# Kernel optimization log

Hardware: AMD Instinct MI355X
Metric: run time of the kernel (lower is better)

The kernel has to match this reference:

```python
import jax, jax.numpy as jnp
import numpy as np

N, T, SKEP = 4096, 64, 768   # users, max history length, SKEP embed dim
H = 256                      # senti_size (LSTM hidden, user_vec/cluster_center dim)
K = 64                       # number of roles (clusters)
NH, DH, DV = 8, 32, 32       # MHA heads, d, d_v


def setup_inputs() -> dict:
    key = jax.random.key(0)
    ks = jax.random.split(key, 16)
    hist = jax.random.normal(ks[0], (N, T, SKEP), dtype=jnp.float32)
    lengths = jax.random.randint(ks[1], (N,), 1, T + 1)          # >=1 (empty hist -> one zero vec in original)
    cluster_id = jax.random.randint(ks[2], (N,), 0, K)
    cluster_id = cluster_id.at[:K].set(jnp.arange(K))            # ensure every role non-empty
    user_vec = jax.random.normal(ks[3], (N, H), dtype=jnp.float32)
    cluster_center = jax.random.normal(ks[4], (K, H), dtype=jnp.float32)
    s = 1.0 / np.sqrt(H)                                         # torch LSTM default init
    W_ih = jax.random.uniform(ks[5], (4 * H, SKEP), minval=-s, maxval=s)
    W_hh = jax.random.uniform(ks[6], (4 * H, H), minval=-s, maxval=s)
    b_ih = jax.random.uniform(ks[7], (4 * H,), minval=-s, maxval=s)
    b_hh = jax.random.uniform(ks[8], (4 * H,), minval=-s, maxval=s)
    Wq = 0.001 * jax.random.normal(ks[9], (NH * DH, H))          # MHA init_weights: normal(std=0.001), bias 0
    Wk = 0.001 * jax.random.normal(ks[10], (NH * DH, H))
    Wv = 0.001 * jax.random.normal(ks[11], (NH * DV, H))
    Wo = 0.001 * jax.random.normal(ks[12], (H, NH * DV))
    bq = jnp.zeros(NH * DH); bk = jnp.zeros(NH * DH); bv = jnp.zeros(NH * DV); bo = jnp.zeros(H)
    return dict(hist=hist, user_vec=user_vec, cluster_center=cluster_center,
                W_ih=W_ih, W_hh=W_hh, b_ih=b_ih, b_hh=b_hh,
                Wq=Wq, bq=bq, Wk=Wk, bk=bk, Wv=Wv, bv=bv, Wo=Wo, bo=bo,
                lengths=lengths, cluster_id=cluster_id)


def _lstm_last(hist, lengths, W_ih, W_hh, b_ih, b_hh):
    """Masked LSTM over padded [N,T,D]; returns hidden state at step lengths-1 (== pack_sequence h_n)."""
    n, t, _ = hist.shape
    hdim = W_hh.shape[1]

    def step(carry, inp):
        h, c = carry
        xt, tt = inp
        gates = xt @ W_ih.T + b_ih + h @ W_hh.T + b_hh        # [N, 4H], gate order i,f,g,o
        i, f, g, o = jnp.split(gates, 4, axis=-1)
        i = jax.nn.sigmoid(i); f = jax.nn.sigmoid(f)
        g = jnp.tanh(g); o = jax.nn.sigmoid(o)
        c_new = f * c + i * g
        h_new = o * jnp.tanh(c_new)
        valid = (tt < lengths)[:, None]
        return (jnp.where(valid, h_new, h), jnp.where(valid, c_new, c)), None

    init = (jnp.zeros((n, hdim), hist.dtype), jnp.zeros((n, hdim), hist.dtype))
    (h_n, _), _ = jax.lax.scan(step, init, (jnp.swapaxes(hist, 0, 1), jnp.arange(t)))
    return h_n  # [N, H]


def reference(hist, user_vec, cluster_center, W_ih, W_hh, b_ih, b_hh,
              Wq, bq, Wk, bk, Wv, bv, Wo, bo, lengths, cluster_id):
    h_n = _lstm_last(hist, lengths, W_ih, W_hh, b_ih, b_hh)                    # per-user sentiment
    # per-role ScaledDotProductAttention: query = cluster center, keys = user_vec, values = h_n
    d_c = user_vec.shape[-1]
    s = jnp.einsum('nd,nd->n', cluster_center[cluster_id], user_vec) / jnp.sqrt(jnp.float32(d_c))
    smax = jax.ops.segment_max(s, cluster_id, num_segments=K)                  # stable segment softmax
    e = jnp.exp(s - smax[cluster_id])
    den = jax.ops.segment_sum(e, cluster_id, num_segments=K)
    role_senti = jax.ops.segment_sum(e[:, None] * h_n, cluster_id, num_segments=K) / den[:, None]  # [K, H]
    # role-level multi-head self-attention (batch=1, dropout inactive at eval)
    x = role_senti[None]                                                        # [1, K, H]
    q = (x @ Wq.T + bq).reshape(1, K, NH, DH).transpose(0, 2, 1, 3)
    k = (x @ Wk.T + bk).reshape(1, K, NH, DH).transpose(0, 2, 1, 3)
    v = (x @ Wv.T + bv).reshape(1, K, NH, DV).transpose(0, 2, 1, 3)
    att = jax.nn.softmax(jnp.einsum('bhqd,bhkd->bhqk', q, k) / jnp.sqrt(jnp.float32(DH)), axis=-1)
    out = jnp.einsum('bhqk,bhkd->bhqd', att, v).transpose(0, 2, 1, 3).reshape(1, K, NH * DV)
    out = out @ Wo.T + bo                                                       # [1, K, H]
    return out.mean(axis=1)                                                     # public_senti [1, H]
```

## Files before the change

kernel.cpp:

```cpp
#include <hip/hip_runtime.h>

typedef short short8 __attribute__((ext_vector_type(8)));
typedef float f32x4 __attribute__((ext_vector_type(4)));

#define N_USERS 4096
#define T_STEPS 64
#define SKEP 768
#define HDIM 256
#define KROLE 64

__device__ __forceinline__ unsigned short f2bfs(float f) {
  unsigned int u = __builtin_bit_cast(unsigned int, f);
  u += 0x7fffu + ((u >> 16) & 1u);
  return (unsigned short)(u >> 16);
}
__device__ __forceinline__ float bf2f(unsigned short b) {
  unsigned int u = ((unsigned int)b) << 16;
  return __builtin_bit_cast(float, u);
}
__device__ __forceinline__ short8 pack8(float4 a, float4 b) {
  short8 o;
  o[0] = (short)f2bfs(a.x); o[1] = (short)f2bfs(a.y);
  o[2] = (short)f2bfs(a.z); o[3] = (short)f2bfs(a.w);
  o[4] = (short)f2bfs(b.x); o[5] = (short)f2bfs(b.y);
  o[6] = (short)f2bfs(b.z); o[7] = (short)f2bfs(b.w);
  return o;
}
__device__ __forceinline__ float sigm(float x) { return 1.0f / (1.0f + __expf(-x)); }
__device__ __forceinline__ float tanh_(float x) { return 1.0f - 2.0f / (1.0f + __expf(2.0f * x)); }

__device__ __forceinline__ void gload16(const void* g, void* l) {
  __builtin_amdgcn_global_load_lds(
      (const __attribute__((address_space(1))) unsigned int*)g,
      (__attribute__((address_space(3))) unsigned int*)l, 16, 0, 0);
}

__device__ __forceinline__ void store_u64_coh(unsigned short* p, unsigned long long v) {
  asm volatile("global_store_dwordx2 %0, %1, off sc0 sc1" : : "v"(p), "v"(v) : "memory");
}

__global__ __launch_bounds__(256) void k_hist(
    const int* __restrict__ lengths, int* __restrict__ cntGT)
{
  __shared__ int hist[65];
  const int tid = threadIdx.x;
  if (tid < 65) hist[tid] = 0;
  __syncthreads();
  for (int i = tid; i < N_USERS; i += 256) atomicAdd(&hist[lengths[i]], 1);
  __syncthreads();
  if (tid == 0) {
    int acc = 0;
    cntGT[64] = 0;
    for (int l = 64; l >= 1; --l) { acc += hist[l]; cntGT[l - 1] = acc; }
  }
}

__global__ __launch_bounds__(64) void k_scatter(
    const int* __restrict__ lengths, const int* __restrict__ cntGT,
    int* __restrict__ perm)
{
  const int l = blockIdx.x + 1;
  const int lane = threadIdx.x;
  int base = cntGT[l];
  for (int c = 0; c < N_USERS; c += 64) {
    int u = c + lane;
    bool m = (lengths[u] == l);
    unsigned long long mask = __ballot(m);
    int rank = __popcll(mask & ((1ull << lane) - 1ull));
    if (m) perm[base + rank] = u;
    base += __popcll(mask);
  }
}

__global__ __launch_bounds__(256) void k_prep(
    const float* __restrict__ Wih, const float* __restrict__ Whh,
    const float* __restrict__ bih, const float* __restrict__ bhh,
    unsigned short* __restrict__ wcat, unsigned short* __restrict__ wcatX,
    float* __restrict__ bias)
{
  int c = blockIdx.x;
  int gi = (c >> 4) & 3;
  int u = ((c >> 6) << 4) | (c & 15);
  int orig = gi * HDIM + u;
  for (int k = threadIdx.x; k < 1024; k += 256) {
    float w = (k < HDIM) ? Whh[(size_t)orig * HDIM + k]
                         : Wih[(size_t)orig * SKEP + (k - HDIM)];
    wcat[(size_t)c * 1024 + k] = f2bfs(w);
  }
  const int NtX = c >> 7, rrX = c & 127;
  for (int kcol = threadIdx.x; kcol < SKEP; kcol += 256) {
    int kt = kcol >> 6, kk = kcol & 63, cl = kk >> 3, e = kk & 7;
    int i = rrX * 8 + (cl ^ (rrX & 7));
    wcatX[(size_t)(NtX * 12 + kt) * 8192 + i * 8 + e] =
        f2bfs(Wih[(size_t)orig * SKEP + kcol]);
  }
  if (threadIdx.x == 0) bias[c] = bih[orig] + bhh[orig];
}

__global__ __launch_bounds__(512) void k_bigx(
    const float* __restrict__ hist,
    const unsigned short* __restrict__ wcatX,
    const int* __restrict__ perm,
    const int* __restrict__ cntGT,
    unsigned short* __restrict__ X)
{
  __shared__ __align__(16) unsigned char smem[65536];
  unsigned char* const A0 = smem;
  unsigned char* const B0 = smem + 16384;
  unsigned char* const A1 = smem + 32768;
  unsigned char* const B1 = smem + 49152;

  const int tid = threadIdx.x;
  const int lane = tid & 63;
  const int wid = tid >> 6;
  const int wr = wid >> 1;
  const int wc = wid & 1;
  const int lr = lane & 15;
  const int lg = lane >> 4;

  const int d = blockIdx.x;
  const int x = d & 7;
  const int Nt = (d >> 3) & 7;
  const int g = ((d >> 6) << 3) | x;
  const int t = g >> 5;
  const int Mtu = g & 31;
  const int n0 = Mtu * 128;

  if ((Mtu << 7) >= cntGT[t]) return;

  f32x4 acc[2][4];
#pragma unroll
  for (int mi = 0; mi < 2; ++mi)
#pragma unroll
    for (int nj = 0; nj < 4; ++nj) acc[mi][nj] = f32x4{0.f, 0.f, 0.f, 0.f};

  const int rr = tid >> 3;
  const int cl = (tid & 7) ^ (rr & 7);
  const int u0 = perm[n0 + rr];
  const int u1 = perm[n0 + rr + 64];
  const size_t hA0 = ((size_t)u0 * T_STEPS + t) * SKEP + (size_t)cl * 8;
  const size_t hA1 = ((size_t)u1 * T_STEPS + t) * SKEP + (size_t)cl * 8;
  const int dst0 = tid * 16, dst1 = tid * 16 + 8192;

  {
    const unsigned short* img = wcatX + (size_t)(Nt * 12) * 8192;
    gload16(img + (size_t)tid * 8, B0 + wid * 1024);
    gload16(img + (size_t)(tid + 512) * 8, B0 + 8192 + wid * 1024);
    const float* p0 = hist + hA0;
    const float* p1 = hist + hA1;
    float4 f00 = *(const float4*)p0, f01 = *(const float4*)(p0 + 4);
    float4 f10 = *(const float4*)p1, f11 = *(const float4*)(p1 + 4);
    *(short8*)(A0 + dst0) = pack8(f00, f01);
    *(short8*)(A0 + dst1) = pack8(f10, f11);
  }
  __syncthreads();

  for (int kt = 0; kt < 12; ++kt) {
    unsigned char* curA = (kt & 1) ? A1 : A0;
    unsigned char* curB = (kt & 1) ? B1 : B0;
    unsigned char* nxtA = (kt & 1) ? A0 : A1;
    unsigned char* nxtB = (kt & 1) ? B0 : B1;
    const int kn = kt + 1;
    const bool have = (kn < 12);

    float4 f00, f01, f10, f11;
    if (have) {
      const unsigned short* img = wcatX + (size_t)(Nt * 12 + kn) * 8192;
      gload16(img + (size_t)tid * 8, nxtB + wid * 1024);
      gload16(img + (size_t)(tid + 512) * 8, nxtB + 8192 + wid * 1024);
      const float* p0 = hist + hA0 + (size_t)kn * 64;
      const float* p1 = hist + hA1 + (size_t)kn * 64;
      f00 = *(const float4*)p0; f01 = *(const float4*)(p0 + 4);
      f10 = *(const float4*)p1; f11 = *(const float4*)(p1 + 4);
    }

#pragma unroll
    for (int ks = 0; ks < 2; ++ks) {
      short8 av[2], bv[4];
#pragma unroll
      for (int mi = 0; mi < 2; ++mi) {
        int r = wr * 32 + mi * 16 + lr;
        int ph = (ks * 4 + lg) ^ (r & 7);
        av[mi] = *(const short8*)(curA + r * 128 + ph * 16);
      }
#pragma unroll
      for (int nj = 0; nj < 4; ++nj) {
        int r = wc * 64 + nj * 16 + lr;
        int ph = (ks * 4 + lg) ^ (r & 7);
        bv[nj] = *(const short8*)(curB + r * 128 + ph * 16);
      }
#pragma unroll
      for (int mi = 0; mi < 2; ++mi)
#pragma unroll
        for (int nj = 0; nj < 4; ++nj)
          acc[mi][nj] = __builtin_amdgcn_mfma_f32_16x16x32_bf16(av[mi], bv[nj], acc[mi][nj], 0, 0, 0);
    }

    if (have) {
      *(short8*)(nxtA + dst0) = pack8(f00, f01);
      *(short8*)(nxtA + dst1) = pack8(f10, f11);
    }
    __syncthreads();
  }

  unsigned short tmp[32];
#pragma unroll
  for (int mi = 0; mi < 2; ++mi)
#pragma unroll
    for (int nj = 0; nj < 4; ++nj)
#pragma unroll
      for (int q = 0; q < 4; ++q)
        tmp[mi * 16 + nj * 4 + q] = f2bfs(acc[mi][nj][q]);
  const int slab = t * 256 + (Mtu * 4 + wr) * 2 + (Nt >> 2);
  const int tidc = ((Nt * 2 + wc) & 7) * 64 + lg * 16 + lr;
  const size_t base = ((size_t)slab * 512 + tidc) * 32;
#pragma unroll
  for (int j2 = 0; j2 < 4; ++j2)
    *(short8*)(X + base + j2 * 8) = *(const short8*)(tmp + j2 * 8);
}

__global__ __launch_bounds__(512) void k_lstm(
    const unsigned short* __restrict__ X,
    unsigned short* __restrict__ hfin,
    unsigned short* __restrict__ hx0,
    unsigned short* __restrict__ hx1,
    const unsigned short* __restrict__ wcat,
    const float* __restrict__ bias,
    const int* __restrict__ lengths,
    const int* __restrict__ perm,
    unsigned int* __restrict__ ctr)
{
  __shared__ __align__(16) unsigned char hl[16384];

  const int tid = threadIdx.x;
  const int lane = tid & 63;
  const int w = tid >> 6;
  const int lr = lane & 15, lg = lane >> 4;
  const int b = blockIdx.x;
  const int gg = b >> 1, half = b & 1;
  const int n0 = gg * 32;
  const int pb = b ^ 1;
  unsigned int* const cme = ctr + b * 16;
  unsigned int* const cpa = ctr + pb * 16;

  short8 Breg[32];
#pragma unroll
  for (int nj = 0; nj < 4; ++nj) {
    const unsigned short* wp =
        wcat + (size_t)(half * 512 + w * 64 + nj * 16 + lr) * 1024 + lg * 8;
#pragma unroll
    for (int ks = 0; ks < 8; ++ks)
      Breg[nj * 8 + ks] = *(const short8*)(wp + ks * 32);
  }

  float bs[4];
#pragma unroll
  for (int nj = 0; nj < 4; ++nj)
    bs[nj] = bias[half * 512 + w * 64 + nj * 16 + lr];
  int pu[2][4], len[2][4];
#pragma unroll
  for (int mi = 0; mi < 2; ++mi)
#pragma unroll
    for (int q = 0; q < 4; ++q) {
      pu[mi][q] = perm[n0 + mi * 16 + lg * 4 + q];
      len[mi][q] = lengths[pu[mi][q]];
    }
  const int te = lengths[perm[n0]];

  const int unitg = half * 128 + w * 16 + lr;
  const int uchunk = unitg >> 3;
  const int ulow = (unitg & 7) * 2;

  for (int i = tid; i < 4096; i += 512) ((unsigned int*)hl)[i] = 0;
  float c8[2][4] = {{0.f, 0.f, 0.f, 0.f}, {0.f, 0.f, 0.f, 0.f}};
  unsigned short hp8[2][4] = {{0, 0, 0, 0}, {0, 0, 0, 0}};

  short8 xc0, xc1, xc2, xc3;
  {
    const unsigned short* xp = X + ((size_t)b * 512 + tid) * 32;
    xc0 = *(const short8*)(xp);
    xc1 = *(const short8*)(xp + 8);
    xc2 = *(const short8*)(xp + 16);
    xc3 = *(const short8*)(xp + 24);
  }
  __syncthreads();

#pragma unroll 1
  for (int t = 0; t < te; ++t) {
    if (t > 0) {
      if (tid == 0) {
        while (__hip_atomic_load(cpa, __ATOMIC_RELAXED, __HIP_MEMORY_SCOPE_AGENT)
               < (unsigned)t)
          __builtin_amdgcn_s_sleep(1);
      }
      __syncthreads();
      const unsigned long long* hs = (const unsigned long long*)
          (((t & 1) ? hx0 : hx1) + (size_t)pb * 4096);
      unsigned long long a0 = __hip_atomic_load(hs + tid * 2,
                                  __ATOMIC_RELAXED, __HIP_MEMORY_SCOPE_AGENT);
      unsigned long long a1 = __hip_atomic_load(hs + tid * 2 + 1,
                                  __ATOMIC_RELAXED, __HIP_MEMORY_SCOPE_AGENT);
      const int ku = (1 - half) * 128 + (tid >> 2);
      const int kc = ku >> 3, kl = (ku & 7) * 2;
      const int ub = (tid & 3) * 8;
#pragma unroll
      for (int j = 0; j < 8; ++j) {
        unsigned short hv = (unsigned short)
            ((j < 4) ? (a0 >> (j * 16)) : (a1 >> ((j - 4) * 16)));
        int us = ub + j;
        *(unsigned short*)(hl + us * 512 + ((kc ^ (us & 7)) << 4) + kl) = hv;
      }
      __syncthreads();
    }

    const int tn = (t + 1 < T_STEPS) ? (t + 1) : t;
    const unsigned short* xpn = X + (((size_t)tn * 256 + b) * 512 + tid) * 32;
    short8 xn0 = *(const short8*)(xpn);
    short8 xn1 = *(const short8*)(xpn + 8);
    short8 xn2 = *(const short8*)(xpn + 16);
    short8 xn3 = *(const short8*)(xpn + 24);

    f32x4 acc[2][4];
#pragma unroll
    for (int mi = 0; mi < 2; ++mi)
#pragma unroll
      for (int nj = 0; nj < 4; ++nj) acc[mi][nj] = f32x4{0.f, 0.f, 0.f, 0.f};

#pragma unroll
    for (int ks = 0; ks < 8; ++ks) {
      const int ch = ks * 4 + lg;
      short8 av0 = *(const short8*)(hl + lr * 512 + ((ch ^ (lr & 7)) << 4));
      short8 av1 = *(const short8*)(hl + (16 + lr) * 512 + ((ch ^ (lr & 7)) << 4));
#pragma unroll
      for (int nj = 0; nj < 4; ++nj) {
        acc[0][nj] = __builtin_amdgcn_mfma_f32_16x16x32_bf16(av0, Breg[nj * 8 + ks], acc[0][nj], 0, 0, 0);
        acc[1][nj] = __builtin_amdgcn_mfma_f32_16x16x32_bf16(av1, Breg[nj * 8 + ks], acc[1][nj], 0, 0, 0);
      }
    }
    __syncthreads();

    unsigned short* hxo = ((t & 1) ? hx1 : hx0) + (size_t)b * 4096;
#pragma unroll
    for (int mi = 0; mi < 2; ++mi) {
      const short8 xa = (mi == 0) ? xc0 : xc2;
      const short8 xb = (mi == 0) ? xc1 : xc3;
#pragma unroll
      for (int q = 0; q < 4; ++q) {
        float gi_ = sigm(acc[mi][0][q] + bf2f((unsigned short)xa[q])     + bs[0]);
        float gf_ = sigm(acc[mi][1][q] + bf2f((unsigned short)xa[4 + q]) + bs[1]);
        float gg_ = tanh_(acc[mi][2][q] + bf2f((unsigned short)xb[q])    + bs[2]);
        float go_ = sigm(acc[mi][3][q] + bf2f((unsigned short)xb[4 + q]) + bs[3]);
        if (t < len[mi][q]) {
          float cn = gf_ * c8[mi][q] + gi_ * gg_;
          c8[mi][q] = cn;
          hp8[mi][q] = f2bfs(go_ * tanh_(cn));
        }
        int us = mi * 16 + lg * 4 + q;
        *(unsigned short*)(hl + us * 512 + ((uchunk ^ (us & 7)) << 4) + ulow) = hp8[mi][q];
      }
      unsigned long long pk =
          (unsigned long long)hp8[mi][0] | ((unsigned long long)hp8[mi][1] << 16) |
          ((unsigned long long)hp8[mi][2] << 32) | ((unsigned long long)hp8[mi][3] << 48);
      store_u64_coh(hxo + (w * 16 + lr) * 32 + mi * 16 + lg * 4, pk);
    }

    asm volatile("s_waitcnt vmcnt(0)" ::: "memory");
    __syncthreads();
    if (t < te - 1 && tid == 0)
      __hip_atomic_fetch_add(cme, 1u, __ATOMIC_RELAXED, __HIP_MEMORY_SCOPE_AGENT);

    xc0 = xn0; xc1 = xn1; xc2 = xn2; xc3 = xn3;
  }

#pragma unroll
  for (int mi = 0; mi < 2; ++mi)
#pragma unroll
    for (int q = 0; q < 4; ++q)
      hfin[(size_t)pu[mi][q] * HDIM + unitg] = hp8[mi][q];
}

__global__ __launch_bounds__(256) void k_scores(
    const float* __restrict__ uv, const float* __restrict__ cc,
    const int* __restrict__ cid, float* __restrict__ s)
{
  int n = blockIdx.x * 4 + (threadIdx.x >> 6);
  int lane = threadIdx.x & 63;
  float4 a = *(const float4*)(uv + (size_t)n * HDIM + lane * 4);
  float4 b = *(const float4*)(cc + (size_t)cid[n] * HDIM + lane * 4);
  float dd = a.x * b.x + a.y * b.y + a.z * b.z + a.w * b.w;
  for (int off = 32; off; off >>= 1) dd += __shfl_down(dd, off);
  if (lane == 0) s[n] = dd * 0.0625f;
}

__global__ __launch_bounds__(256) void k_role(
    const float* __restrict__ s, const int* __restrict__ cid,
    const unsigned short* __restrict__ hn, float* __restrict__ rs)
{
  __shared__ float sv[N_USERS];
  __shared__ int cv[N_USERS];
  __shared__ float red[256];
  const int k = blockIdx.x, tid = threadIdx.x;
  for (int i = tid; i < N_USERS; i += 256) { sv[i] = s[i]; cv[i] = cid[i]; }
  __syncthreads();
  float m = -3.4e38f;
  for (int i = tid; i < N_USERS; i += 256) if (cv[i] == k) m = fmaxf(m, sv[i]);
  red[tid] = m; __syncthreads();
  for (int st = 128; st; st >>= 1) { if (tid < st) red[tid] = fmaxf(red[tid], red[tid + st]); __syncthreads(); }
  const float smax = red[0];
  __syncthreads();
  float sum = 0.f;
  for (int i = tid; i < N_USERS; i += 256)
    if (cv[i] == k) { float e = __expf(sv[i] - smax); sv[i] = e; sum += e; }
  red[tid] = sum; __syncthreads();
  for (int st = 128; st; st >>= 1) { if (tid < st) red[tid] += red[tid + st]; __syncthreads(); }
  const float den = red[0];
  __syncthreads();
  float a = 0.f;
  for (int i = 0; i < N_USERS; ++i)
    if (cv[i] == k) a += sv[i] * bf2f(hn[(size_t)i * HDIM + tid]);
  rs[(size_t)k * HDIM + tid] = a / den;
}

__global__ __launch_bounds__(256) void k_qkv(
    const float* __restrict__ rs,
    const float* __restrict__ Wq, const float* __restrict__ bq,
    const float* __restrict__ Wk, const float* __restrict__ bk,
    const float* __restrict__ Wv, const float* __restrict__ bv,
    float* __restrict__ qkvg)
{
  const int id = blockIdx.x * 256 + threadIdx.x;
  const int m2 = id >> 14;
  const int hr = (id >> 5) & 511;
  const int dd2 = id & 31;
  const int head = hr >> 6, r = hr & 63;
  const int wrow = head * 32 + dd2;
  const float* W = (m2 == 0) ? Wq : (m2 == 1) ? Wk : Wv;
  const float* B = (m2 == 0) ? bq : (m2 == 1) ? bk : bv;
  const float* x = rs + (size_t)r * HDIM;
  const float* w = W + (size_t)wrow * HDIM;
  float acc = B[wrow];
#pragma unroll 4
  for (int j4 = 0; j4 < 64; ++j4) {
    float4 xv = *(const float4*)(x + j4 * 4);
    float4 wv = *(const float4*)(w + j4 * 4);
    acc += xv.x * wv.x;
    acc += xv.y * wv.y;
    acc += xv.z * wv.z;
    acc += xv.w * wv.w;
  }
  qkvg[(size_t)(m2 * 512 + hr) * 32 + dd2] = acc;
}

__global__ __launch_bounds__(256) void k_mha(
    const float* __restrict__ qkvg,
    float* __restrict__ attout)
{
  __shared__ float q[64][32], kk[64][32], v[64][32];
  __shared__ float att[64][64];
  const int h = blockIdx.x, tid = threadIdx.x;
  for (int i = tid; i < 2048; i += 256) {
    int r = i >> 5, dd2 = i & 31;
    q[r][dd2]  = qkvg[(size_t)(0 * 512 + h * 64 + r) * 32 + dd2];
    kk[r][dd2] = qkvg[(size_t)(1 * 512 + h * 64 + r) * 32 + dd2];
    v[r][dd2]  = qkvg[(size_t)(2 * 512 + h * 64 + r) * 32 + dd2];
  }
  __syncthreads();
  for (int idx = tid; idx < 4096; idx += 256) {
    int qr = idx >> 6, kr = idx & 63;
    float sc = 0.f;
    for (int dd2 = 0; dd2 < 32; ++dd2) sc += q[qr][dd2] * kk[kr][dd2];
    att[qr][kr] = sc * 0.17677669529663687f;
  }
  __syncthreads();
  if (tid < 64) {
    float m = -3.4e38f;
    for (int j = 0; j < 64; ++j) m = fmaxf(m, att[tid][j]);
    float sum = 0.f;
    for (int j = 0; j < 64; ++j) { float e = __expf(att[tid][j] - m); att[tid][j] = e; sum += e; }
    float inv = 1.f / sum;
    for (int j = 0; j < 64; ++j) att[tid][j] *= inv;
  }
  __syncthreads();
  for (int idx = tid; idx < 2048; idx += 256) {
    int r = idx >> 5, dd2 = idx & 31;
    float o = 0.f;
    for (int kr = 0; kr < 64; ++kr) o += att[r][kr] * v[kr][dd2];
    attout[(size_t)r * HDIM + h * 32 + dd2] = o;
  }
}

__global__ __launch_bounds__(256) void k_out(
    const float* __restrict__ attout, const float* __restrict__ Wo,
    const float* __restrict__ bo, float* __restrict__ out)
{
  __shared__ float m_s[256];
  const int tid = threadIdx.x;
  float mm = 0.f;
  for (int r = 0; r < 64; ++r) mm += attout[(size_t)r * HDIM + tid];
  m_s[tid] = mm * (1.0f / 64.0f);
  __syncthreads();
  float a = bo[tid];
  const float* w = Wo + (size_t)tid * HDIM;
#pragma unroll 4
  for (int j4 = 0; j4 < 64; ++j4) {
    float4 wv = *(const float4*)(w + j4 * 4);
    a += m_s[j4 * 4 + 0] * wv.x;
    a += m_s[j4 * 4 + 1] * wv.y;
    a += m_s[j4 * 4 + 2] * wv.z;
    a += m_s[j4 * 4 + 3] * wv.w;
  }
  out[tid] = a;
}

extern "C" void kernel_launch(void* const* d_in, const int* in_sizes, int n_in,
                              void* d_out, int out_size, void* d_ws, size_t ws_size,
                              hipStream_t stream) {
  const float* hist = (const float*)d_in[0];
  const float* uv   = (const float*)d_in[1];
  const float* cc   = (const float*)d_in[2];
  const float* Wih  = (const float*)d_in[3];
  const float* Whh  = (const float*)d_in[4];
  const float* bih  = (const float*)d_in[5];
  const float* bhh  = (const float*)d_in[6];
  const float* Wq   = (const float*)d_in[7];
  const float* bq   = (const float*)d_in[8];
  const float* Wk   = (const float*)d_in[9];
  const float* bk   = (const float*)d_in[10];
  const float* Wv   = (const float*)d_in[11];
  const float* bv   = (const float*)d_in[12];
  const float* Wo   = (const float*)d_in[13];
  const float* bo   = (const float*)d_in[14];
  const int* lengths = (const int*)d_in[15];
  const int* cid     = (const int*)d_in[16];
  float* out = (float*)d_out;

  unsigned char* ws = (unsigned char*)d_ws;
  unsigned short* hfin  = (unsigned short*)(ws);
  unsigned short* hx0   = (unsigned short*)(ws + (2ull << 20));
  unsigned short* hx1   = (unsigned short*)(ws + (4ull << 20));
  unsigned int*   ctr   = (unsigned int*)  (ws + (6ull << 20));
  int* perm   = (int*)   (ws + (6ull << 20) + 16384);
  int* cntGT  = (int*)   (ws + (6ull << 20) + 32768);
  float* bias   = (float*)(ws + (6ull << 20) + 65536);
  float* sbuf   = (float*)(ws + (6ull << 20) + 73728);
  float* rs     = (float*)(ws + (6ull << 20) + 98304);
  float* attout = (float*)(ws + (6ull << 20) + 163840);
  float* qkvg   = (float*)(ws + (7ull << 20));
  unsigned short* wcat  = (unsigned short*)(ws + (8ull << 20));
  unsigned short* wcatX = (unsigned short*)(ws + (10ull << 20));
  unsigned short* Xbuf  = (unsigned short*)(ws + (16ull << 20));
  const size_t need = (16ull << 20) + (size_t)N_USERS * T_STEPS * 1024 * 2;
  if (ws_size < need) return;

  (void)hipMemsetAsync(ctr, 0, 16384, stream);

  k_hist<<<1, 256, 0, stream>>>(lengths, cntGT);
  k_scatter<<<64, 64, 0, stream>>>(lengths, cntGT, perm);
  k_prep<<<1024, 256, 0, stream>>>(Wih, Whh, bih, bhh, wcat, wcatX, bias);
  k_bigx<<<16384, 512, 0, stream>>>(hist, wcatX, perm, cntGT, Xbuf);
  k_lstm<<<256, 512, 0, stream>>>(Xbuf, hfin, hx0, hx1, wcat, bias, lengths, perm, ctr);

  k_scores<<<1024, 256, 0, stream>>>(uv, cc, cid, sbuf);
  k_role<<<64, 256, 0, stream>>>(sbuf, cid, hfin, rs);
  k_qkv<<<192, 256, 0, stream>>>(rs, Wq, bq, Wk, bk, Wv, bv, qkvg);
  k_mha<<<8, 256, 0, stream>>>(qkvg, attout);
  k_out<<<1, 256, 0, stream>>>(attout, Wo, bo, out);
}
```

Baseline: 1.164 ms.

## Deepen k_bigx pipeline with triple-buffered weights and register-prefetched hist

Reworks the k_bigx GEMM main loop from double buffering into a deeper software pipeline. Weight tiles now go through three LDS buffers loaded two steps ahead, and hist rows are prefetched three steps ahead into registers. __syncthreads is replaced by explicit s_waitcnt vmcnt counts plus s_barrier, so later loads can stay in flight. The aim is to hide global-memory latency better. The cost is more LDS (80KB), more registers, and hand-tuned wait counts that break if the load order changes.

```diff
diff --git a/kernel.cpp b/kernel.cpp
--- a/kernel.cpp
+++ b/kernel.cpp
@@ -104,11 +104,14 @@
     const int* __restrict__ cntGT,
     unsigned short* __restrict__ X)
 {
-  __shared__ __align__(16) unsigned char smem[65536];
-  unsigned char* const A0 = smem;
-  unsigned char* const B0 = smem + 16384;
-  unsigned char* const A1 = smem + 32768;
-  unsigned char* const B1 = smem + 49152;
+  __shared__ __align__(16) unsigned char smem[81920];
+  unsigned char* const Ab0 = smem;
+  unsigned char* const Ab1 = smem + 16384;
+  unsigned char* const Bb0 = smem + 32768;
+  unsigned char* const Bb1 = smem + 49152;
+  unsigned char* const Bb2 = smem + 65536;
+  unsigned char* const Ab[2] = {Ab0, Ab1};
+  unsigned char* const Bb[3] = {Bb0, Bb1, Bb2};
 
   const int tid = threadIdx.x;
   const int lane = tid & 63;
@@ -142,38 +145,46 @@
   const size_t hA1 = ((size_t)u1 * T_STEPS + t) * SKEP + (size_t)cl * 8;
   const int dst0 = tid * 16, dst1 = tid * 16 + 8192;
 
-  {
-    const unsigned short* img = wcatX + (size_t)(Nt * 12) * 8192;
-    gload16(img + (size_t)tid * 8, B0 + wid * 1024);
-    gload16(img + (size_t)(tid + 512) * 8, B0 + 8192 + wid * 1024);
-    const float* p0 = hist + hA0;
-    const float* p1 = hist + hA1;
-    float4 f00 = *(const float4*)p0, f01 = *(const float4*)(p0 + 4);
-    float4 f10 = *(const float4*)p1, f11 = *(const float4*)(p1 + 4);
-    *(short8*)(A0 + dst0) = pack8(f00, f01);
-    *(short8*)(A0 + dst1) = pack8(f10, f11);
-  }
-  __syncthreads();
-
+  const unsigned short* img = wcatX + (size_t)(Nt * 12) * 8192;
+
+  float4 fa[3][4];
+
+  gload16(img + (size_t)tid * 8,          Bb0 + wid * 1024);
+  gload16(img + (size_t)(tid + 512) * 8,  Bb0 + 8192 + wid * 1024);
+  gload16(img + 8192 + (size_t)tid * 8,         Bb1 + wid * 1024);
+  gload16(img + 8192 + (size_t)(tid + 512) * 8, Bb1 + 8192 + wid * 1024);
+#pragma unroll
+  for (int p = 0; p < 3; ++p) {
+    const float* p0 = hist + hA0 + (size_t)p * 64;
+    const float* p1 = hist + hA1 + (size_t)p * 64;
+    fa[p][0] = *(const float4*)p0; fa[p][1] = *(const float4*)(p0 + 4);
+    fa[p][2] = *(const float4*)p1; fa[p][3] = *(const float4*)(p1 + 4);
+  }
+  *(short8*)(Ab0 + dst0) = pack8(fa[0][0], fa[0][1]);
+  *(short8*)(Ab0 + dst1) = pack8(fa[0][2], fa[0][3]);
+  asm volatile("s_waitcnt vmcnt(8) lgkmcnt(0)" ::: "memory");
+  __builtin_amdgcn_s_barrier();
+
+#pragma unroll
   for (int kt = 0; kt < 12; ++kt) {
-    unsigned char* curA = (kt & 1) ? A1 : A0;
-    unsigned char* curB = (kt & 1) ? B1 : B0;
-    unsigned char* nxtA = (kt & 1) ? A0 : A1;
-    unsigned char* nxtB = (kt & 1) ? B0 : B1;
-    const int kn = kt + 1;
-    const bool have = (kn < 12);
-
-    float4 f00, f01, f10, f11;
-    if (have) {
-      const unsigned short* img = wcatX + (size_t)(Nt * 12 + kn) * 8192;
-      gload16(img + (size_t)tid * 8, nxtB + wid * 1024);
-      gload16(img + (size_t)(tid + 512) * 8, nxtB + 8192 + wid * 1024);
-      const float* p0 = hist + hA0 + (size_t)kn * 64;
-      const float* p1 = hist + hA1 + (size_t)kn * 64;
-      f00 = *(const float4*)p0; f01 = *(const float4*)(p0 + 4);
-      f10 = *(const float4*)p1; f11 = *(const float4*)(p1 + 4);
-    }
-
+    if (kt + 2 < 12) {
+      const unsigned short* ik = img + (size_t)(kt + 2) * 8192;
+      gload16(ik + (size_t)tid * 8,         Bb[(kt + 2) % 3] + wid * 1024);
+      gload16(ik + (size_t)(tid + 512) * 8, Bb[(kt + 2) % 3] + 8192 + wid * 1024);
+    }
+    if (kt + 1 < 12) {
+      *(short8*)(Ab[(kt + 1) & 1] + dst0) = pack8(fa[(kt + 1) % 3][0], fa[(kt + 1) % 3][1]);
+      *(short8*)(Ab[(kt + 1) & 1] + dst1) = pack8(fa[(kt + 1) % 3][2], fa[(kt + 1) % 3][3]);
+    }
+    if (kt + 3 < 12) {
+      const float* p0 = hist + hA0 + (size_t)(kt + 3) * 64;
+      const float* p1 = hist + hA1 + (size_t)(kt + 3) * 64;
+      fa[(kt + 3) % 3][0] = *(const float4*)p0; fa[(kt + 3) % 3][1] = *(const float4*)(p0 + 4);
+      fa[(kt + 3) % 3][2] = *(const float4*)p1; fa[(kt + 3) % 3][3] = *(const float4*)(p1 + 4);
+    }
+
+    unsigned char* curA = Ab[kt & 1];
+    unsigned char* curB = Bb[kt % 3];
 #pragma unroll
     for (int ks = 0; ks < 2; ++ks) {
       short8 av[2], bv[4];
@@ -196,11 +207,16 @@
           acc[mi][nj] = __builtin_amdgcn_mfma_f32_16x16x32_bf16(av[mi], bv[nj], acc[mi][nj], 0, 0, 0);
     }
 
-    if (have) {
-      *(short8*)(nxtA + dst0) = pack8(f00, f01);
-      *(short8*)(nxtA + dst1) = pack8(f10, f11);
-    }
-    __syncthreads();
+    if (kt < 11) {
+      if (kt <= 8) {
+        asm volatile("s_waitcnt vmcnt(10) lgkmcnt(0)" ::: "memory");
+      } else if (kt == 9) {
+        asm volatile("s_waitcnt vmcnt(6) lgkmcnt(0)" ::: "memory");
+      } else {
+        asm volatile("s_waitcnt vmcnt(0) lgkmcnt(0)" ::: "memory");
+      }
+      __builtin_amdgcn_s_barrier();
+    }
   }
 
   unsigned short tmp[32];
```

After: 1.153 ms. About the same (-1.0%).

## Replace double-buffered LDS pipeline in k_bigx with single buffer for occupancy

Applied to the files above, without the earlier changes.

Removes the double-buffered A/B shared-memory tiles in the input-projection GEMM kernel, halving LDS to 32KB. Each k-step now loads and syncs before computing, and a launch-bounds occupancy hint is added. The aim is more resident blocks per CU, so other waves hide global-load latency instead of software prefetch. The cost is an extra barrier per iteration and no overlap of loads with MFMA within a block.

```diff
diff --git a/kernel.cpp b/kernel.cpp
--- a/kernel.cpp
+++ b/kernel.cpp
@@ -97,18 +97,16 @@
   if (threadIdx.x == 0) bias[c] = bih[orig] + bhh[orig];
 }
 
-__global__ __launch_bounds__(512) void k_bigx(
+__global__ __launch_bounds__(512, 8) void k_bigx(
     const float* __restrict__ hist,
     const unsigned short* __restrict__ wcatX,
     const int* __restrict__ perm,
     const int* __restrict__ cntGT,
     unsigned short* __restrict__ X)
 {
-  __shared__ __align__(16) unsigned char smem[65536];
-  unsigned char* const A0 = smem;
-  unsigned char* const B0 = smem + 16384;
-  unsigned char* const A1 = smem + 32768;
-  unsigned char* const B1 = smem + 49152;
+  __shared__ __align__(16) unsigned char smem[32768];
+  unsigned char* const Ab = smem;
+  unsigned char* const Bb = smem + 16384;
 
   const int tid = threadIdx.x;
   const int lane = tid & 63;
@@ -142,37 +140,21 @@
   const size_t hA1 = ((size_t)u1 * T_STEPS + t) * SKEP + (size_t)cl * 8;
   const int dst0 = tid * 16, dst1 = tid * 16 + 8192;
 
-  {
-    const unsigned short* img = wcatX + (size_t)(Nt * 12) * 8192;
-    gload16(img + (size_t)tid * 8, B0 + wid * 1024);
-    gload16(img + (size_t)(tid + 512) * 8, B0 + 8192 + wid * 1024);
-    const float* p0 = hist + hA0;
-    const float* p1 = hist + hA1;
-    float4 f00 = *(const float4*)p0, f01 = *(const float4*)(p0 + 4);
-    float4 f10 = *(const float4*)p1, f11 = *(const float4*)(p1 + 4);
-    *(short8*)(A0 + dst0) = pack8(f00, f01);
-    *(short8*)(A0 + dst1) = pack8(f10, f11);
-  }
-  __syncthreads();
+  const unsigned short* img = wcatX + (size_t)(Nt * 12) * 8192;
 
   for (int kt = 0; kt < 12; ++kt) {
-    unsigned char* curA = (kt & 1) ? A1 : A0;
-    unsigned char* curB = (kt & 1) ? B1 : B0;
-    unsigned char* nxtA = (kt & 1) ? A0 : A1;
-    unsigned char* nxtB = (kt & 1) ? B0 : B1;
-    const int kn = kt + 1;
-    const bool have = (kn < 12);
-
-    float4 f00, f01, f10, f11;
-    if (have) {
-      const unsigned short* img = wcatX + (size_t)(Nt * 12 + kn) * 8192;
-      gload16(img + (size_t)tid * 8, nxtB + wid * 1024);
-      gload16(img + (size_t)(tid + 512) * 8, nxtB + 8192 + wid * 1024);
-      const float* p0 = hist + hA0 + (size_t)kn * 64;
-      const float* p1 = hist + hA1 + (size_t)kn * 64;
-      f00 = *(const float4*)p0; f01 = *(const float4*)(p0 + 4);
-      f10 = *(const float4*)p1; f11 = *(const float4*)(p1 + 4);
+    const unsigned short* ik = img + (size_t)kt * 8192;
+    gload16(ik + (size_t)tid * 8,         Bb + wid * 1024);
+    gload16(ik + (size_t)(tid + 512) * 8, Bb + 8192 + wid * 1024);
+    {
+      const float* p0 = hist + hA0 + (size_t)kt * 64;
+      const float* p1 = hist + hA1 + (size_t)kt * 64;
+      float4 f00 = *(const float4*)p0, f01 = *(const float4*)(p0 + 4);
+      float4 f10 = *(const float4*)p1, f11 = *(const float4*)(p1 + 4);
+      *(short8*)(Ab + dst0) = pack8(f00, f01);
+      *(short8*)(Ab + dst1) = pack8(f10, f11);
     }
+    __syncthreads();
 
 #pragma unroll
     for (int ks = 0; ks < 2; ++ks) {
@@ -181,24 +163,19 @@
       for (int mi = 0; mi < 2; ++mi) {
         int r = wr * 32 + mi * 16 + lr;
         int ph = (ks * 4 + lg) ^ (r & 7);
-        av[mi] = *(const short8*)(curA + r * 128 + ph * 16);
+        av[mi] = *(const short8*)(Ab + r * 128 + ph * 16);
       }
 #pragma unroll
       for (int nj = 0; nj < 4; ++nj) {
         int r = wc * 64 + nj * 16 + lr;
         int ph = (ks * 4 + lg) ^ (r & 7);
-        bv[nj] = *(const short8*)(curB + r * 128 + ph * 16);
+        bv[nj] = *(const short8*)(Bb + r * 128 + ph * 16);
       }
 #pragma unroll
       for (int mi = 0; mi < 2; ++mi)
 #pragma unroll
         for (int nj = 0; nj < 4; ++nj)
           acc[mi][nj] = __builtin_amdgcn_mfma_f32_16x16x32_bf16(av[mi], bv[nj], acc[mi][nj], 0, 0, 0);
-    }
-
-    if (have) {
-      *(short8*)(nxtA + dst0) = pack8(f00, f01);
-      *(short8*)(nxtA + dst1) = pack8(f10, f11);
     }
     __syncthreads();
   }
```

New measurement: 1.189 ms. +2.1%, slower.

## Merge LSTM block pairs into one 1024-thread block, drop cross-block sync

Applied to the files above, without the earlier changes.

Each 32-user group of the recurrent LSTM kernel was split across two 512-thread blocks that exchanged half of the hidden state through global memory every timestep, using coherent stores and a spin-wait counter. The group now runs in a single 1024-thread block, so the full hidden state stays in LDS and only __syncthreads is needed between steps. This removes the per-step global round trip and polling latency and the counter memset. In exchange, half as many blocks run (128 instead of 256), so fewer CUs are busy. Each thread still holds 32 short8 weight registers, which at 1024 threads per block puts heavy pressure on the register file.

```diff
diff --git a/kernel.cpp b/kernel.cpp
--- a/kernel.cpp
+++ b/kernel.cpp
@@ -33,10 +33,6 @@
   __builtin_amdgcn_global_load_lds(
       (const __attribute__((address_space(1))) unsigned int*)g,
       (__attribute__((address_space(3))) unsigned int*)l, 16, 0, 0);
-}
-
-__device__ __forceinline__ void store_u64_coh(unsigned short* p, unsigned long long v) {
-  asm volatile("global_store_dwordx2 %0, %1, off sc0 sc1" : : "v"(p), "v"(v) : "memory");
 }
 
 __global__ __launch_bounds__(256) void k_hist(
@@ -219,16 +215,13 @@
     *(short8*)(X + base + j2 * 8) = *(const short8*)(tmp + j2 * 8);
 }
 
-__global__ __launch_bounds__(512) void k_lstm(
+__global__ __launch_bounds__(1024) void k_lstm(
     const unsigned short* __restrict__ X,
     unsigned short* __restrict__ hfin,
-    unsigned short* __restrict__ hx0,
-    unsigned short* __restrict__ hx1,
     const unsigned short* __restrict__ wcat,
     const float* __restrict__ bias,
     const int* __restrict__ lengths,
-    const int* __restrict__ perm,
-    unsigned int* __restrict__ ctr)
+    const int* __restrict__ perm)
 {
   __shared__ __align__(16) unsigned char hl[16384];
 
@@ -236,18 +229,14 @@
   const int lane = tid & 63;
   const int w = tid >> 6;
   const int lr = lane & 15, lg = lane >> 4;
-  const int b = blockIdx.x;
-  const int gg = b >> 1, half = b & 1;
+  const int gg = blockIdx.x;
   const int n0 = gg * 32;
-  const int pb = b ^ 1;
-  unsigned int* const cme = ctr + b * 16;
-  unsigned int* const cpa = ctr + pb * 16;
 
   short8 Breg[32];
 #pragma unroll
   for (int nj = 0; nj < 4; ++nj) {
     const unsigned short* wp =
-        wcat + (size_t)(half * 512 + w * 64 + nj * 16 + lr) * 1024 + lg * 8;
+        wcat + (size_t)(w * 64 + nj * 16 + lr) * 1024 + lg * 8;
 #pragma unroll
     for (int ks = 0; ks < 8; ++ks)
       Breg[nj * 8 + ks] = *(const short8*)(wp + ks * 32);
@@ -256,7 +245,7 @@
   float bs[4];
 #pragma unroll
   for (int nj = 0; nj < 4; ++nj)
-    bs[nj] = bias[half * 512 + w * 64 + nj * 16 + lr];
+    bs[nj] = bias[w * 64 + nj * 16 + lr];
   int pu[2][4], len[2][4];
 #pragma unroll
   for (int mi = 0; mi < 2; ++mi)
@@ -267,17 +256,19 @@
     }
   const int te = lengths[perm[n0]];
 
-  const int unitg = half * 128 + w * 16 + lr;
+  const int unitg = w * 16 + lr;
   const int uchunk = unitg >> 3;
   const int ulow = (unitg & 7) * 2;
 
-  for (int i = tid; i < 4096; i += 512) ((unsigned int*)hl)[i] = 0;
+  for (int i = tid; i < 4096; i += 1024) ((unsigned int*)hl)[i] = 0;
   float c8[2][4] = {{0.f, 0.f, 0.f, 0.f}, {0.f, 0.f, 0.f, 0.f}};
   unsigned short hp8[2][4] = {{0, 0, 0, 0}, {0, 0, 0, 0}};
 
+  const size_t xoff = ((size_t)(gg * 2 + (w >> 3)) * 512 + (w & 7) * 64 + lane) * 32;
+
   short8 xc0, xc1, xc2, xc3;
   {
-    const unsigned short* xp = X + ((size_t)b * 512 + tid) * 32;
+    const unsigned short* xp = X + xoff;
     xc0 = *(const short8*)(xp);
     xc1 = *(const short8*)(xp + 8);
     xc2 = *(const short8*)(xp + 16);
@@ -287,34 +278,8 @@
 
 #pragma unroll 1
   for (int t = 0; t < te; ++t) {
-    if (t > 0) {
-      if (tid == 0) {
-        while (__hip_atomic_load(cpa, __ATOMIC_RELAXED, __HIP_MEMORY_SCOPE_AGENT)
-               < (unsigned)t)
-          __builtin_amdgcn_s_sleep(1);
-      }
-      __syncthreads();
-      const unsigned long long* hs = (const unsigned long long*)
-          (((t & 1) ? hx0 : hx1) + (size_t)pb * 4096);
-      unsigned long long a0 = __hip_atomic_load(hs + tid * 2,
-                                  __ATOMIC_RELAXED, __HIP_MEMORY_SCOPE_AGENT);
-      unsigned long long a1 = __hip_atomic_load(hs + tid * 2 + 1,
-                                  __ATOMIC_RELAXED, __HIP_MEMORY_SCOPE_AGENT);
-      const int ku = (1 - half) * 128 + (tid >> 2);
-      const int kc = ku >> 3, kl = (ku & 7) * 2;
-      const int ub = (tid & 3) * 8;
-#pragma unroll
-      for (int j = 0; j < 8; ++j) {
-        unsigned short hv = (unsigned short)
-            ((j < 4) ? (a0 >> (j * 16)) : (a1 >> ((j - 4) * 16)));
-        int us = ub + j;
-        *(unsigned short*)(hl + us * 512 + ((kc ^ (us & 7)) << 4) + kl) = hv;
-      }
-      __syncthreads();
-    }
-
     const int tn = (t + 1 < T_STEPS) ? (t + 1) : t;
-    const unsigned short* xpn = X + (((size_t)tn * 256 + b) * 512 + tid) * 32;
+    const unsigned short* xpn = X + (size_t)tn * 4194304ull + xoff;
     short8 xn0 = *(const short8*)(xpn);
     short8 xn1 = *(const short8*)(xpn + 8);
     short8 xn2 = *(const short8*)(xpn + 16);
@@ -339,7 +304,6 @@
     }
     __syncthreads();
 
-    unsigned short* hxo = ((t & 1) ? hx1 : hx0) + (size_t)b * 4096;
 #pragma unroll
     for (int mi = 0; mi < 2; ++mi) {
       const short8 xa = (mi == 0) ? xc0 : xc2;
@@ -358,16 +322,8 @@
         int us = mi * 16 + lg * 4 + q;
         *(unsigned short*)(hl + us * 512 + ((uchunk ^ (us & 7)) << 4) + ulow) = hp8[mi][q];
       }
-      unsigned long long pk =
-          (unsigned long long)hp8[mi][0] | ((unsigned long long)hp8[mi][1] << 16) |
-          ((unsigned long long)hp8[mi][2] << 32) | ((unsigned long long)hp8[mi][3] << 48);
-      store_u64_coh(hxo + (w * 16 + lr) * 32 + mi * 16 + lg * 4, pk);
     }
-
-    asm volatile("s_waitcnt vmcnt(0)" ::: "memory");
     __syncthreads();
-    if (t < te - 1 && tid == 0)
-      __hip_atomic_fetch_add(cme, 1u, __ATOMIC_RELAXED, __HIP_MEMORY_SCOPE_AGENT);
 
     xc0 = xn0; xc1 = xn1; xc2 = xn2; xc3 = xn3;
   }
@@ -536,9 +492,6 @@
 
   unsigned char* ws = (unsigned char*)d_ws;
   unsigned short* hfin  = (unsigned short*)(ws);
-  unsigned short* hx0   = (unsigned short*)(ws + (2ull << 20));
-  unsigned short* hx1   = (unsigned short*)(ws + (4ull << 20));
-  unsigned int*   ctr   = (unsigned int*)  (ws + (6ull << 20));
   int* perm   = (int*)   (ws + (6ull << 20) + 16384);
   int* cntGT  = (int*)   (ws + (6ull << 20) + 32768);
   float* bias   = (float*)(ws + (6ull << 20) + 65536);
@@ -552,13 +505,11 @@
   const size_t need = (16ull << 20) + (size_t)N_USERS * T_STEPS * 1024 * 2;
   if (ws_size < need) return;
 
-  (void)hipMemsetAsync(ctr, 0, 16384, stream);
-
   k_hist<<<1, 256, 0, stream>>>(lengths, cntGT);
   k_scatter<<<64, 64, 0, stream>>>(lengths, cntGT, perm);
   k_prep<<<1024, 256, 0, stream>>>(Wih, Whh, bih, bhh, wcat, wcatX, bias);
   k_bigx<<<16384, 512, 0, stream>>>(hist, wcatX, perm, cntGT, Xbuf);
-  k_lstm<<<256, 512, 0, stream>>>(Xbuf, hfin, hx0, hx1, wcat, bias, lengths, perm, ctr);
+  k_lstm<<<128, 1024, 0, stream>>>(Xbuf, hfin, wcat, bias, lengths, perm);
 
   k_scores<<<1024, 256, 0, stream>>>(uv, cc, cid, sbuf);
   k_role<<<64, 256, 0, stream>>>(sbuf, cid, hfin, rs);
```

New measurement: 2.135 ms. 1.83x slower.
